# Kernel optimization log

Hardware: AMD Instinct MI355X
Metric: run time of the kernel (lower is better)

## Reference

```python
import jax, jax.numpy as jnp
import numpy as np

H, T, D = 16, 4096, 64
N_SEQ = 8  # packed sequences -> cu_seqlens has N_SEQ+1 entries


def setup_inputs() -> dict:
    key = jax.random.key(0)
    kq, kk, kv, kc = jax.random.split(key, 4)
    q = jax.random.normal(kq, (1, H, T, D), dtype=jnp.float32)
    k = jax.random.normal(kk, (1, H, T, D), dtype=jnp.float32)
    v = jax.random.normal(kv, (1, H, T, D), dtype=jnp.float32)
    # cu_seqlens: monotonically increasing offsets, starts at 0, ends at T
    interior = jnp.sort(jax.random.randint(kc, (N_SEQ - 1,), 1, T, dtype=jnp.int32))
    cu_seqlens = jnp.concatenate([
        jnp.zeros((1,), jnp.int32), interior, jnp.full((1,), T, jnp.int32)
    ])
    return {"q": q, "k": k, "v": v, "cu_seqlens": cu_seqlens}


def reference(q, k, v, cu_seqlens):
    # Faithful to flash_attn_varlen_func(..., causal=False) on packed sequences:
    # non-causal attention restricted block-diagonally to each segment.
    scale = 1.0 / jnp.sqrt(jnp.asarray(D, q.dtype))
    # segment id for every token position
    pos = jnp.arange(T)
    seg = jnp.searchsorted(cu_seqlens[1:], pos, side="right")  # [T]
    mask = seg[:, None] == seg[None, :]                         # [T, T] block-diagonal
    # scores: [1, H, T, T]
    scores = jnp.einsum("bhqd,bhkd->bhqk", q, k) * scale
    neg = jnp.asarray(jnp.finfo(scores.dtype).min, scores.dtype)
    scores = jnp.where(mask[None, None], scores, neg)
    attn = jax.nn.softmax(scores, axis=-1)
    out = jnp.einsum("bhqk,bhkd->bhqd", attn, v)  # [1, H, T, D]
    return out
```

## Files before the change

### kernel.cpp

```cpp
#include <hip/hip_runtime.h>

#define HH 16
#define TT 4096
#define DD 64

typedef __attribute__((ext_vector_type(2))) __fp16 half2r;
typedef __attribute__((ext_vector_type(4))) _Float16 half4;
typedef __attribute__((ext_vector_type(8))) _Float16 half8;
typedef __attribute__((ext_vector_type(2))) float float2v;
typedef __attribute__((ext_vector_type(4))) float float4v;

__global__ __launch_bounds__(256, 4) void pa_fwd(
    const float* __restrict__ qg, const float* __restrict__ kg,
    const float* __restrict__ vg, const int* __restrict__ cu,
    float* __restrict__ outg)
{
    __shared__ __align__(16) _Float16 Kl[2][64 * 64];
    __shared__ __align__(16) _Float16 Vl[2][64 * 64];

    const int tid  = threadIdx.x;
    const int lane = tid & 63;
    const int wave = tid >> 6;
    const int lr   = lane & 15;
    const int lg   = lane >> 4;

    const int bswz = ((int)blockIdx.x & 7) * 128 + ((int)blockIdx.x >> 3);
    const int h    = bswz >> 6;
    const int qblk = (bswz & 63) << 6;
    const int q    = qblk + wave * 16 + lr;

    int s = 0;
    while (cu[s + 1] <= q) ++s;
    const int lo = cu[s], hi = cu[s + 1];

    int sb = 0;
    while (cu[sb + 1] <= qblk) ++sb;
    const int blo = cu[sb];
    while (cu[sb + 1] <= qblk + 63) ++sb;
    const int bhi = cu[sb + 1];

    const int wlo = __shfl(lo, 0);
    const int whi = __shfl(hi, 15);
    const int mlo = __shfl(lo, 15);
    const int mhi = __shfl(hi, 0);

    const float qscale = 0.125f * 1.44269504088896f;
    const float* qrow = qg + ((size_t)h * TT + q) * DD;
    half8 qf8[2];
#pragma unroll
    for (int ds = 0; ds < 2; ++ds) {
        const float* qp = qrow + ds * 32 + lg * 8;
        float4v a = *(const float4v*)qp;
        float4v b = *(const float4v*)(qp + 4);
        half2r p0 = __builtin_amdgcn_cvt_pkrtz(a[0] * qscale, a[1] * qscale);
        half2r p1 = __builtin_amdgcn_cvt_pkrtz(a[2] * qscale, a[3] * qscale);
        half2r p2 = __builtin_amdgcn_cvt_pkrtz(b[0] * qscale, b[1] * qscale);
        half2r p3 = __builtin_amdgcn_cvt_pkrtz(b[2] * qscale, b[3] * qscale);
        qf8[ds][0] = (_Float16)p0[0]; qf8[ds][1] = (_Float16)p0[1];
        qf8[ds][2] = (_Float16)p1[0]; qf8[ds][3] = (_Float16)p1[1];
        qf8[ds][4] = (_Float16)p2[0]; qf8[ds][5] = (_Float16)p2[1];
        qf8[ds][6] = (_Float16)p3[0]; qf8[ds][7] = (_Float16)p3[1];
    }

    const float* kh_ = kg + (size_t)h * TT * DD;
    const float* vh_ = vg + (size_t)h * TT * DD;

    const int srow = tid >> 2;
    const int sc   = tid & 3;
    const unsigned kwrA = (unsigned)(srow * 128 + (((2 * sc)     ^ (srow & 7)) << 4));
    const unsigned kwrB = (unsigned)(srow * 128 + (((2 * sc + 1) ^ (srow & 7)) << 4));
    const int vd2 = tid & 31;
    const int vko = tid >> 5;
    const int vr0 = 2 * vd2, vr1 = 2 * vd2 + 1;
    const unsigned vwrA = (unsigned)(vr0 * 128 + ((vko ^ (vr0 & 7)) << 4));
    const unsigned vwrB = (unsigned)(vr1 * 128 + ((vko ^ (vr1 & 7)) << 4));

    const unsigned kb0 = (unsigned)(lr * 128 + (((lg)     ^ (lr & 7)) << 4));
    const unsigned kb1 = (unsigned)(lr * 128 + (((4 + lg) ^ (lr & 7)) << 4));
    unsigned vrb[4];
#pragma unroll
    for (int t = 0; t < 4; ++t)
        vrb[t] = (unsigned)(lr * 128 + (((2 * t + (lg >> 1)) ^ (lr & 7)) << 4) +
                            ((lg & 1) << 3));

    half4 onesv;
    onesv[0] = onesv[1] = onesv[2] = onesv[3] = (_Float16)1.0f;

    float4v kq[4];
    float2v vv2[8];
    const int t0k = blo & ~63;
    const float4v* kp = (const float4v*)(kh_ + (size_t)(t0k + srow) * DD + sc * 16);
    const float*   vp = vh_ + (size_t)(t0k + vko * 8) * DD + vd2 * 2;

#define ISSUE()                                                                \
    {                                                                          \
        kq[0] = kp[0]; kq[1] = kp[1]; kq[2] = kp[2]; kq[3] = kp[3];            \
        kp += (64 * DD) / 4;                                                   \
        _Pragma("unroll")                                                      \
        for (int c = 0; c < 8; ++c) vv2[c] = *(const float2v*)(vp + c * DD);   \
        vp += 64 * DD;                                                         \
    }

    ISSUE();

    float4v acc[4];
#pragma unroll
    for (int dt = 0; dt < 4; ++dt) acc[dt] = (float4v){0.f, 0.f, 0.f, 0.f};
    float4v acc_l = (float4v){0.f, 0.f, 0.f, 0.f};
    float m_run = -1e30f;

    int cur = 0;
    for (int kt = t0k; kt < bhi; kt += 64) {
        {
            char* Kb = (char*)Kl[cur];
            char* Vb = (char*)Vl[cur];
            half8 hk0, hk1, hv0, hv1;
#pragma unroll
            for (int i = 0; i < 2; ++i) {
                half2r a = __builtin_amdgcn_cvt_pkrtz(kq[i][0], kq[i][1]);
                half2r b = __builtin_amdgcn_cvt_pkrtz(kq[i][2], kq[i][3]);
                hk0[4 * i + 0] = (_Float16)a[0]; hk0[4 * i + 1] = (_Float16)a[1];
                hk0[4 * i + 2] = (_Float16)b[0]; hk0[4 * i + 3] = (_Float16)b[1];
                half2r c2 = __builtin_amdgcn_cvt_pkrtz(kq[2 + i][0], kq[2 + i][1]);
                half2r d2 = __builtin_amdgcn_cvt_pkrtz(kq[2 + i][2], kq[2 + i][3]);
                hk1[4 * i + 0] = (_Float16)c2[0]; hk1[4 * i + 1] = (_Float16)c2[1];
                hk1[4 * i + 2] = (_Float16)d2[0]; hk1[4 * i + 3] = (_Float16)d2[1];
            }
#pragma unroll
            for (int i = 0; i < 4; ++i) {
                half2r a = __builtin_amdgcn_cvt_pkrtz(vv2[2 * i][0], vv2[2 * i + 1][0]);
                half2r b = __builtin_amdgcn_cvt_pkrtz(vv2[2 * i][1], vv2[2 * i + 1][1]);
                hv0[2 * i] = (_Float16)a[0]; hv0[2 * i + 1] = (_Float16)a[1];
                hv1[2 * i] = (_Float16)b[0]; hv1[2 * i + 1] = (_Float16)b[1];
            }
            *(half8*)(Kb + kwrA) = hk0;
            *(half8*)(Kb + kwrB) = hk1;
            *(half8*)(Vb + vwrA) = hv0;
            *(half8*)(Vb + vwrB) = hv1;
        }
        __syncthreads();

        if (kt + 64 < bhi) ISSUE();

        if (!(kt + 64 <= wlo || kt >= whi)) {
            const char* Kb = (const char*)Kl[cur];
            const char* Vb = (const char*)Vl[cur];

            float st[4][4];
            const bool fullv = (kt >= mlo) && (kt + 64 <= mhi);
            __builtin_amdgcn_s_setprio(1);
#pragma unroll
            for (int t = 0; t < 4; ++t) {
                float4v sa = (float4v){0.f, 0.f, 0.f, 0.f};
                half8 kf0 = *(const half8*)(Kb + kb0 + t * 2048);
                half8 kf1 = *(const half8*)(Kb + kb1 + t * 2048);
                sa = __builtin_amdgcn_mfma_f32_16x16x32_f16(kf0, qf8[0], sa, 0, 0, 0);
                sa = __builtin_amdgcn_mfma_f32_16x16x32_f16(kf1, qf8[1], sa, 0, 0, 0);
                if (fullv) {
#pragma unroll
                    for (int j = 0; j < 4; ++j) st[t][j] = sa[j];
                } else {
#pragma unroll
                    for (int j = 0; j < 4; ++j) {
                        const int key = kt + t * 16 + lg * 4 + j;
                        st[t][j] = (key >= lo && key < hi) ? sa[j] : -1e30f;
                    }
                }
            }
            __builtin_amdgcn_s_setprio(0);

            float lmax = fmaxf(fmaxf(st[0][0], st[0][1]), fmaxf(st[0][2], st[0][3]));
            lmax = fmaxf(lmax, fmaxf(fmaxf(st[1][0], st[1][1]), fmaxf(st[1][2], st[1][3])));
            lmax = fmaxf(lmax, fmaxf(fmaxf(st[2][0], st[2][1]), fmaxf(st[2][2], st[2][3])));
            lmax = fmaxf(lmax, fmaxf(fmaxf(st[3][0], st[3][1]), fmaxf(st[3][2], st[3][3])));

            if (__any(lmax > m_run + 11.54f)) {
                float tx = fmaxf(lmax, __shfl_xor(lmax, 16));
                tx = fmaxf(tx, __shfl_xor(tx, 32));
                const float mn = fmaxf(m_run, tx);
                const float a  = exp2f(m_run - mn);
#pragma unroll
                for (int dt = 0; dt < 4; ++dt)
#pragma unroll
                    for (int j = 0; j < 4; ++j) acc[dt][j] *= a;
#pragma unroll
                for (int j = 0; j < 4; ++j) acc_l[j] *= a;
                m_run = mn;
            }

            half4 pb[4];
#pragma unroll
            for (int t = 0; t < 4; ++t) {
                float e0 = exp2f(st[t][0] - m_run);
                float e1 = exp2f(st[t][1] - m_run);
                float e2 = exp2f(st[t][2] - m_run);
                float e3 = exp2f(st[t][3] - m_run);
                half2r a = __builtin_amdgcn_cvt_pkrtz(e0, e1);
                half2r b = __builtin_amdgcn_cvt_pkrtz(e2, e3);
                pb[t][0] = (_Float16)a[0]; pb[t][1] = (_Float16)a[1];
                pb[t][2] = (_Float16)b[0]; pb[t][3] = (_Float16)b[1];
            }

            __builtin_amdgcn_s_setprio(1);
#pragma unroll
            for (int t = 0; t < 4; ++t) {
#pragma unroll
                for (int dt = 0; dt < 4; ++dt) {
                    half4 vf = *(const half4*)(Vb + vrb[t] + dt * 2048);
                    acc[dt] = __builtin_amdgcn_mfma_f32_16x16x16f16(vf, pb[t], acc[dt], 0, 0, 0);
                }
                acc_l = __builtin_amdgcn_mfma_f32_16x16x16f16(onesv, pb[t], acc_l, 0, 0, 0);
            }
            __builtin_amdgcn_s_setprio(0);
        }
        cur ^= 1;
    }

    const float inv = 1.0f / acc_l[0];
    float* orow = outg + ((size_t)h * TT + q) * DD;
#pragma unroll
    for (int dt = 0; dt < 4; ++dt) {
        float4v o;
#pragma unroll
        for (int j = 0; j < 4; ++j) o[j] = acc[dt][j] * inv;
        *(float4v*)(orow + dt * 16 + lg * 4) = o;
    }
#undef ISSUE
}

extern "C" void kernel_launch(void* const* d_in, const int* in_sizes, int n_in,
                              void* d_out, int out_size, void* d_ws, size_t ws_size,
                              hipStream_t stream) {
    const float* q  = (const float*)d_in[0];
    const float* k  = (const float*)d_in[1];
    const float* v  = (const float*)d_in[2];
    const int*   cu = (const int*)d_in[3];
    float* out = (float*)d_out;

    dim3 grid(HH * (TT / 64));
    dim3 block(256);
    hipLaunchKernelGGL(pa_fwd, grid, block, 0, stream, q, k, v, cu, out);
}
```

Measured before the change: 85.65 us.

## Restructure V global loads and LDS layout, prefetch half of V fragments early

The V staging now has each thread load single scalars at column vd2 and vd2+32 rather than float2 pairs, packs them into half4 chunks, and writes them with a new swizzle that also XORs the 8-byte half-slot by a row bit. The V fragment read offsets are updated to match. The first two V fragment groups are read from LDS before the softmax math so their latency overlaps with the exp and max work. This trades wider global loads for narrower scalar ones and adds register pressure for the prefetched fragments, which may matter at 4 blocks per CU.

Result: faster. 81.31 us (-5.1%).

```diff
diff --git a/kernel.cpp b/kernel.cpp
--- a/kernel.cpp
+++ b/kernel.cpp
@@ -7,7 +7,6 @@
 typedef __attribute__((ext_vector_type(2))) __fp16 half2r;
 typedef __attribute__((ext_vector_type(4))) _Float16 half4;
 typedef __attribute__((ext_vector_type(8))) _Float16 half8;
-typedef __attribute__((ext_vector_type(2))) float float2v;
 typedef __attribute__((ext_vector_type(4))) float float4v;
 
 __global__ __launch_bounds__(256, 4) void pa_fwd(
@@ -71,9 +70,12 @@
     const unsigned kwrB = (unsigned)(srow * 128 + (((2 * sc + 1) ^ (srow & 7)) << 4));
     const int vd2 = tid & 31;
     const int vko = tid >> 5;
-    const int vr0 = 2 * vd2, vr1 = 2 * vd2 + 1;
-    const unsigned vwrA = (unsigned)(vr0 * 128 + ((vko ^ (vr0 & 7)) << 4));
-    const unsigned vwrB = (unsigned)(vr1 * 128 + ((vko ^ (vr1 & 7)) << 4));
+    const int vslot = vko ^ (vd2 & 7);
+    const int vhb   = (vd2 >> 3) & 1;
+    const unsigned vwA0 = (unsigned)(vd2 * 128 + vslot * 16 + 8 * vhb);
+    const unsigned vwA1 = (unsigned)(vd2 * 128 + vslot * 16 + 8 * (1 ^ vhb));
+    const unsigned vwB0 = vwA0 + 32 * 128;
+    const unsigned vwB1 = vwA1 + 32 * 128;
 
     const unsigned kb0 = (unsigned)(lr * 128 + (((lg)     ^ (lr & 7)) << 4));
     const unsigned kb1 = (unsigned)(lr * 128 + (((4 + lg) ^ (lr & 7)) << 4));
@@ -81,23 +83,26 @@
 #pragma unroll
     for (int t = 0; t < 4; ++t)
         vrb[t] = (unsigned)(lr * 128 + (((2 * t + (lg >> 1)) ^ (lr & 7)) << 4) +
-                            ((lg & 1) << 3));
+                            (((lg & 1) ^ ((lr >> 3) & 1)) << 3));
 
     half4 onesv;
     onesv[0] = onesv[1] = onesv[2] = onesv[3] = (_Float16)1.0f;
 
     float4v kq[4];
-    float2v vv2[8];
+    float vvA[8], vvB[8];
     const int t0k = blo & ~63;
     const float4v* kp = (const float4v*)(kh_ + (size_t)(t0k + srow) * DD + sc * 16);
-    const float*   vp = vh_ + (size_t)(t0k + vko * 8) * DD + vd2 * 2;
+    const float*   vp = vh_ + (size_t)(t0k + vko * 8) * DD + vd2;
 
 #define ISSUE()                                                                \
     {                                                                          \
         kq[0] = kp[0]; kq[1] = kp[1]; kq[2] = kp[2]; kq[3] = kp[3];            \
         kp += (64 * DD) / 4;                                                   \
         _Pragma("unroll")                                                      \
-        for (int c = 0; c < 8; ++c) vv2[c] = *(const float2v*)(vp + c * DD);   \
+        for (int c = 0; c < 8; ++c) {                                          \
+            vvA[c] = vp[c * DD];                                               \
+            vvB[c] = vp[c * DD + 32];                                          \
+        }                                                                      \
         vp += 64 * DD;                                                         \
     }
 
@@ -114,7 +119,7 @@
         {
             char* Kb = (char*)Kl[cur];
             char* Vb = (char*)Vl[cur];
-            half8 hk0, hk1, hv0, hv1;
+            half8 hk0, hk1;
 #pragma unroll
             for (int i = 0; i < 2; ++i) {
                 half2r a = __builtin_amdgcn_cvt_pkrtz(kq[i][0], kq[i][1]);
@@ -126,17 +131,32 @@
                 hk1[4 * i + 0] = (_Float16)c2[0]; hk1[4 * i + 1] = (_Float16)c2[1];
                 hk1[4 * i + 2] = (_Float16)d2[0]; hk1[4 * i + 3] = (_Float16)d2[1];
             }
-#pragma unroll
-            for (int i = 0; i < 4; ++i) {
-                half2r a = __builtin_amdgcn_cvt_pkrtz(vv2[2 * i][0], vv2[2 * i + 1][0]);
-                half2r b = __builtin_amdgcn_cvt_pkrtz(vv2[2 * i][1], vv2[2 * i + 1][1]);
-                hv0[2 * i] = (_Float16)a[0]; hv0[2 * i + 1] = (_Float16)a[1];
-                hv1[2 * i] = (_Float16)b[0]; hv1[2 * i + 1] = (_Float16)b[1];
-            }
             *(half8*)(Kb + kwrA) = hk0;
             *(half8*)(Kb + kwrB) = hk1;
-            *(half8*)(Vb + vwrA) = hv0;
-            *(half8*)(Vb + vwrB) = hv1;
+
+            half4 uA0, uA1, uB0, uB1;
+            {
+                half2r a = __builtin_amdgcn_cvt_pkrtz(vvA[0], vvA[1]);
+                half2r b = __builtin_amdgcn_cvt_pkrtz(vvA[2], vvA[3]);
+                uA0[0] = (_Float16)a[0]; uA0[1] = (_Float16)a[1];
+                uA0[2] = (_Float16)b[0]; uA0[3] = (_Float16)b[1];
+                half2r c2 = __builtin_amdgcn_cvt_pkrtz(vvA[4], vvA[5]);
+                half2r d2 = __builtin_amdgcn_cvt_pkrtz(vvA[6], vvA[7]);
+                uA1[0] = (_Float16)c2[0]; uA1[1] = (_Float16)c2[1];
+                uA1[2] = (_Float16)d2[0]; uA1[3] = (_Float16)d2[1];
+                half2r e = __builtin_amdgcn_cvt_pkrtz(vvB[0], vvB[1]);
+                half2r f = __builtin_amdgcn_cvt_pkrtz(vvB[2], vvB[3]);
+                uB0[0] = (_Float16)e[0]; uB0[1] = (_Float16)e[1];
+                uB0[2] = (_Float16)f[0]; uB0[3] = (_Float16)f[1];
+                half2r g = __builtin_amdgcn_cvt_pkrtz(vvB[4], vvB[5]);
+                half2r k2 = __builtin_amdgcn_cvt_pkrtz(vvB[6], vvB[7]);
+                uB1[0] = (_Float16)g[0]; uB1[1] = (_Float16)g[1];
+                uB1[2] = (_Float16)k2[0]; uB1[3] = (_Float16)k2[1];
+            }
+            *(half4*)(Vb + vwA0) = uA0;
+            *(half4*)(Vb + vwA1) = uA1;
+            *(half4*)(Vb + vwB0) = uB0;
+            *(half4*)(Vb + vwB1) = uB1;
         }
         __syncthreads();
 
@@ -168,6 +188,13 @@
                 }
             }
             __builtin_amdgcn_s_setprio(0);
+
+            half4 vf01[2][4];
+#pragma unroll
+            for (int t = 0; t < 2; ++t)
+#pragma unroll
+                for (int dt = 0; dt < 4; ++dt)
+                    vf01[t][dt] = *(const half4*)(Vb + vrb[t] + dt * 2048);
 
             float lmax = fmaxf(fmaxf(st[0][0], st[0][1]), fmaxf(st[0][2], st[0][3]));
             lmax = fmaxf(lmax, fmaxf(fmaxf(st[1][0], st[1][1]), fmaxf(st[1][2], st[1][3])));
@@ -203,7 +230,14 @@
 
             __builtin_amdgcn_s_setprio(1);
 #pragma unroll
-            for (int t = 0; t < 4; ++t) {
+            for (int t = 0; t < 2; ++t) {
+#pragma unroll
+                for (int dt = 0; dt < 4; ++dt)
+                    acc[dt] = __builtin_amdgcn_mfma_f32_16x16x16f16(vf01[t][dt], pb[t], acc[dt], 0, 0, 0);
+                acc_l = __builtin_amdgcn_mfma_f32_16x16x16f16(onesv, pb[t], acc_l, 0, 0, 0);
+            }
+#pragma unroll
+            for (int t = 2; t < 4; ++t) {
 #pragma unroll
                 for (int dt = 0; dt < 4; ++dt) {
                     half4 vf = *(const half4*)(Vb + vrb[t] + dt * 2048);
```

## Software-pipeline QK of next tile with softmax/PV of current tile

Applied to the files above, without the earlier changes.

Restructures the main loop so the QK^T MFMAs for tile kt+64 are issued before the softmax and PV work for tile kt, with scores carried across iterations. This exposes more independent MFMA work per wave to hide latency. It also changes the V global load and LDS write pattern to scalar loads with a new half-swizzled layout, and relaxes launch bounds from 4 to 2 blocks per CU to allow more registers. The cost is higher register pressure, possibly lower occupancy, and an extra barrier per iteration.

Measured after the change: 95.06 us. 11.0% more time.

```diff
diff --git a/kernel.cpp b/kernel.cpp
--- a/kernel.cpp
+++ b/kernel.cpp
@@ -7,10 +7,9 @@
 typedef __attribute__((ext_vector_type(2))) __fp16 half2r;
 typedef __attribute__((ext_vector_type(4))) _Float16 half4;
 typedef __attribute__((ext_vector_type(8))) _Float16 half8;
-typedef __attribute__((ext_vector_type(2))) float float2v;
 typedef __attribute__((ext_vector_type(4))) float float4v;
 
-__global__ __launch_bounds__(256, 4) void pa_fwd(
+__global__ __launch_bounds__(256, 2) void pa_fwd(
     const float* __restrict__ qg, const float* __restrict__ kg,
     const float* __restrict__ vg, const int* __restrict__ cu,
     float* __restrict__ outg)
@@ -71,9 +70,12 @@
     const unsigned kwrB = (unsigned)(srow * 128 + (((2 * sc + 1) ^ (srow & 7)) << 4));
     const int vd2 = tid & 31;
     const int vko = tid >> 5;
-    const int vr0 = 2 * vd2, vr1 = 2 * vd2 + 1;
-    const unsigned vwrA = (unsigned)(vr0 * 128 + ((vko ^ (vr0 & 7)) << 4));
-    const unsigned vwrB = (unsigned)(vr1 * 128 + ((vko ^ (vr1 & 7)) << 4));
+    const int vslot = vko ^ (vd2 & 7);
+    const int vhb   = (vd2 >> 3) & 1;
+    const unsigned vwA0 = (unsigned)(vd2 * 128 + vslot * 16 + 8 * vhb);
+    const unsigned vwA1 = (unsigned)(vd2 * 128 + vslot * 16 + 8 * (1 ^ vhb));
+    const unsigned vwB0 = vwA0 + 32 * 128;
+    const unsigned vwB1 = vwA1 + 32 * 128;
 
     const unsigned kb0 = (unsigned)(lr * 128 + (((lg)     ^ (lr & 7)) << 4));
     const unsigned kb1 = (unsigned)(lr * 128 + (((4 + lg) ^ (lr & 7)) << 4));
@@ -81,27 +83,98 @@
 #pragma unroll
     for (int t = 0; t < 4; ++t)
         vrb[t] = (unsigned)(lr * 128 + (((2 * t + (lg >> 1)) ^ (lr & 7)) << 4) +
-                            ((lg & 1) << 3));
+                            (((lg & 1) ^ ((lr >> 3) & 1)) << 3));
 
     half4 onesv;
     onesv[0] = onesv[1] = onesv[2] = onesv[3] = (_Float16)1.0f;
 
     float4v kq[4];
-    float2v vv2[8];
-    const int t0k = blo & ~63;
+    float vvA[8], vvB[8];
+    const int t0k  = blo & ~63;
+    const int tend = bhi;
     const float4v* kp = (const float4v*)(kh_ + (size_t)(t0k + srow) * DD + sc * 16);
-    const float*   vp = vh_ + (size_t)(t0k + vko * 8) * DD + vd2 * 2;
+    const float*   vp = vh_ + (size_t)(t0k + vko * 8) * DD + vd2;
 
 #define ISSUE()                                                                \
     {                                                                          \
         kq[0] = kp[0]; kq[1] = kp[1]; kq[2] = kp[2]; kq[3] = kp[3];            \
         kp += (64 * DD) / 4;                                                   \
         _Pragma("unroll")                                                      \
-        for (int c = 0; c < 8; ++c) vv2[c] = *(const float2v*)(vp + c * DD);   \
+        for (int c = 0; c < 8; ++c) {                                          \
+            vvA[c] = vp[c * DD];                                               \
+            vvB[c] = vp[c * DD + 32];                                          \
+        }                                                                      \
         vp += 64 * DD;                                                         \
     }
 
-    ISSUE();
+#define PACKW(CUR)                                                             \
+    {                                                                          \
+        char* Kb = (char*)Kl[CUR];                                             \
+        char* Vb = (char*)Vl[CUR];                                             \
+        half8 hk0, hk1;                                                        \
+        _Pragma("unroll")                                                      \
+        for (int i = 0; i < 2; ++i) {                                          \
+            half2r a = __builtin_amdgcn_cvt_pkrtz(kq[i][0], kq[i][1]);         \
+            half2r b = __builtin_amdgcn_cvt_pkrtz(kq[i][2], kq[i][3]);         \
+            hk0[4*i+0] = (_Float16)a[0]; hk0[4*i+1] = (_Float16)a[1];          \
+            hk0[4*i+2] = (_Float16)b[0]; hk0[4*i+3] = (_Float16)b[1];          \
+            half2r c2 = __builtin_amdgcn_cvt_pkrtz(kq[2+i][0], kq[2+i][1]);    \
+            half2r d2 = __builtin_amdgcn_cvt_pkrtz(kq[2+i][2], kq[2+i][3]);    \
+            hk1[4*i+0] = (_Float16)c2[0]; hk1[4*i+1] = (_Float16)c2[1];        \
+            hk1[4*i+2] = (_Float16)d2[0]; hk1[4*i+3] = (_Float16)d2[1];        \
+        }                                                                      \
+        *(half8*)(Kb + kwrA) = hk0;                                            \
+        *(half8*)(Kb + kwrB) = hk1;                                            \
+        half4 uA0, uA1, uB0, uB1;                                              \
+        {                                                                      \
+            half2r a = __builtin_amdgcn_cvt_pkrtz(vvA[0], vvA[1]);             \
+            half2r b = __builtin_amdgcn_cvt_pkrtz(vvA[2], vvA[3]);             \
+            uA0[0] = (_Float16)a[0]; uA0[1] = (_Float16)a[1];                  \
+            uA0[2] = (_Float16)b[0]; uA0[3] = (_Float16)b[1];                  \
+            half2r c2 = __builtin_amdgcn_cvt_pkrtz(vvA[4], vvA[5]);            \
+            half2r d2 = __builtin_amdgcn_cvt_pkrtz(vvA[6], vvA[7]);            \
+            uA1[0] = (_Float16)c2[0]; uA1[1] = (_Float16)c2[1];                \
+            uA1[2] = (_Float16)d2[0]; uA1[3] = (_Float16)d2[1];                \
+            half2r e = __builtin_amdgcn_cvt_pkrtz(vvB[0], vvB[1]);             \
+            half2r f = __builtin_amdgcn_cvt_pkrtz(vvB[2], vvB[3]);             \
+            uB0[0] = (_Float16)e[0]; uB0[1] = (_Float16)e[1];                  \
+            uB0[2] = (_Float16)f[0]; uB0[3] = (_Float16)f[1];                  \
+            half2r g = __builtin_amdgcn_cvt_pkrtz(vvB[4], vvB[5]);             \
+            half2r k2 = __builtin_amdgcn_cvt_pkrtz(vvB[6], vvB[7]);            \
+            uB1[0] = (_Float16)g[0]; uB1[1] = (_Float16)g[1];                  \
+            uB1[2] = (_Float16)k2[0]; uB1[3] = (_Float16)k2[1];                \
+        }                                                                      \
+        *(half4*)(Vb + vwA0) = uA0;                                            \
+        *(half4*)(Vb + vwA1) = uA1;                                            \
+        *(half4*)(Vb + vwB0) = uB0;                                            \
+        *(half4*)(Vb + vwB1) = uB1;                                            \
+    }
+
+#define QKM(KT, BUF, ST, VALID)                                                \
+    if (VALID) {                                                               \
+        const char* Kb_ = (const char*)Kl[BUF];                                \
+        const bool fullv_ = ((KT) >= mlo) && ((KT) + 64 <= mhi);               \
+        __builtin_amdgcn_s_setprio(1);                                         \
+        _Pragma("unroll")                                                      \
+        for (int t = 0; t < 4; ++t) {                                          \
+            float4v sa = (float4v){0.f, 0.f, 0.f, 0.f};                        \
+            half8 kf0 = *(const half8*)(Kb_ + kb0 + t * 2048);                 \
+            half8 kf1 = *(const half8*)(Kb_ + kb1 + t * 2048);                 \
+            sa = __builtin_amdgcn_mfma_f32_16x16x32_f16(kf0, qf8[0], sa, 0, 0, 0); \
+            sa = __builtin_amdgcn_mfma_f32_16x16x32_f16(kf1, qf8[1], sa, 0, 0, 0); \
+            if (fullv_) {                                                      \
+                _Pragma("unroll")                                              \
+                for (int j = 0; j < 4; ++j) ST[t][j] = sa[j];                  \
+            } else {                                                           \
+                _Pragma("unroll")                                              \
+                for (int j = 0; j < 4; ++j) {                                  \
+                    const int key = (KT) + t * 16 + lg * 4 + j;                \
+                    ST[t][j] = (key >= lo && key < hi) ? sa[j] : -1e30f;       \
+                }                                                              \
+            }                                                                  \
+        }                                                                      \
+        __builtin_amdgcn_s_setprio(0);                                         \
+    }
 
     float4v acc[4];
 #pragma unroll
@@ -109,65 +182,28 @@
     float4v acc_l = (float4v){0.f, 0.f, 0.f, 0.f};
     float m_run = -1e30f;
 
+    ISSUE();
+    PACKW(0);
+    if (t0k + 64 < tend) ISSUE();
+    __syncthreads();
+    float st[4][4];
+    bool cv = !(t0k + 64 <= wlo || t0k >= whi);
+    QKM(t0k, 0, st, cv);
+
     int cur = 0;
-    for (int kt = t0k; kt < bhi; kt += 64) {
-        {
-            char* Kb = (char*)Kl[cur];
-            char* Vb = (char*)Vl[cur];
-            half8 hk0, hk1, hv0, hv1;
-#pragma unroll
-            for (int i = 0; i < 2; ++i) {
-                half2r a = __builtin_amdgcn_cvt_pkrtz(kq[i][0], kq[i][1]);
-                half2r b = __builtin_amdgcn_cvt_pkrtz(kq[i][2], kq[i][3]);
-                hk0[4 * i + 0] = (_Float16)a[0]; hk0[4 * i + 1] = (_Float16)a[1];
-                hk0[4 * i + 2] = (_Float16)b[0]; hk0[4 * i + 3] = (_Float16)b[1];
-                half2r c2 = __builtin_amdgcn_cvt_pkrtz(kq[2 + i][0], kq[2 + i][1]);
-                half2r d2 = __builtin_amdgcn_cvt_pkrtz(kq[2 + i][2], kq[2 + i][3]);
-                hk1[4 * i + 0] = (_Float16)c2[0]; hk1[4 * i + 1] = (_Float16)c2[1];
-                hk1[4 * i + 2] = (_Float16)d2[0]; hk1[4 * i + 3] = (_Float16)d2[1];
-            }
-#pragma unroll
-            for (int i = 0; i < 4; ++i) {
-                half2r a = __builtin_amdgcn_cvt_pkrtz(vv2[2 * i][0], vv2[2 * i + 1][0]);
-                half2r b = __builtin_amdgcn_cvt_pkrtz(vv2[2 * i][1], vv2[2 * i + 1][1]);
-                hv0[2 * i] = (_Float16)a[0]; hv0[2 * i + 1] = (_Float16)a[1];
-                hv1[2 * i] = (_Float16)b[0]; hv1[2 * i + 1] = (_Float16)b[1];
-            }
-            *(half8*)(Kb + kwrA) = hk0;
-            *(half8*)(Kb + kwrB) = hk1;
-            *(half8*)(Vb + vwrA) = hv0;
-            *(half8*)(Vb + vwrB) = hv1;
-        }
+    for (int kt = t0k; kt < tend; kt += 64) {
         __syncthreads();
-
-        if (kt + 64 < bhi) ISSUE();
-
-        if (!(kt + 64 <= wlo || kt >= whi)) {
-            const char* Kb = (const char*)Kl[cur];
+        if (kt + 64 < tend) PACKW(cur ^ 1);
+        if (kt + 128 < tend) ISSUE();
+        __syncthreads();
+
+        const bool nxv = (kt + 64 < tend) &&
+                         !(kt + 128 <= wlo || kt + 64 >= whi);
+        float stn[4][4];
+        QKM(kt + 64, cur ^ 1, stn, nxv);
+
+        if (cv) {
             const char* Vb = (const char*)Vl[cur];
-
-            float st[4][4];
-            const bool fullv = (kt >= mlo) && (kt + 64 <= mhi);
-            __builtin_amdgcn_s_setprio(1);
-#pragma unroll
-            for (int t = 0; t < 4; ++t) {
-                float4v sa = (float4v){0.f, 0.f, 0.f, 0.f};
-                half8 kf0 = *(const half8*)(Kb + kb0 + t * 2048);
-                half8 kf1 = *(const half8*)(Kb + kb1 + t * 2048);
-                sa = __builtin_amdgcn_mfma_f32_16x16x32_f16(kf0, qf8[0], sa, 0, 0, 0);
-                sa = __builtin_amdgcn_mfma_f32_16x16x32_f16(kf1, qf8[1], sa, 0, 0, 0);
-                if (fullv) {
-#pragma unroll
-                    for (int j = 0; j < 4; ++j) st[t][j] = sa[j];
-                } else {
-#pragma unroll
-                    for (int j = 0; j < 4; ++j) {
-                        const int key = kt + t * 16 + lg * 4 + j;
-                        st[t][j] = (key >= lo && key < hi) ? sa[j] : -1e30f;
-                    }
-                }
-            }
-            __builtin_amdgcn_s_setprio(0);
 
             float lmax = fmaxf(fmaxf(st[0][0], st[0][1]), fmaxf(st[0][2], st[0][3]));
             lmax = fmaxf(lmax, fmaxf(fmaxf(st[1][0], st[1][1]), fmaxf(st[1][2], st[1][3])));
@@ -213,6 +249,14 @@
             }
             __builtin_amdgcn_s_setprio(0);
         }
+
+        if (nxv) {
+#pragma unroll
+            for (int t = 0; t < 4; ++t)
+#pragma unroll
+                for (int j = 0; j < 4; ++j) st[t][j] = stn[t][j];
+        }
+        cv = nxv;
         cur ^= 1;
     }
 
@@ -226,6 +270,8 @@
         *(float4v*)(orow + dt * 16 + lg * 4) = o;
     }
 #undef ISSUE
+#undef PACKW
+#undef QKM
 }
 
 extern "C" void kernel_launch(void* const* d_in, const int* in_sizes, int n_in,
```

## Precompute swizzled fp16 K/V in a prep kernel and stream it into LDS

Applied to the files above, without the earlier changes.

Adds a prep kernel that converts K and V from fp32 to fp16 once. It writes them to workspace already in the swizzled LDS tile layout, with V transposed. The attention kernel then copies 16-byte chunks straight into shared memory, with no per-tile conversion and half the bytes per K/V tile load. The first half of the V fragments is also loaded before the softmax so the LDS reads overlap the exp work. The cost is an extra kernel launch and a workspace write and read pass.

Result: faster. 80.64 us (-5.8%).

```diff
diff --git a/kernel.cpp b/kernel.cpp
--- a/kernel.cpp
+++ b/kernel.cpp
@@ -7,12 +7,83 @@
 typedef __attribute__((ext_vector_type(2))) __fp16 half2r;
 typedef __attribute__((ext_vector_type(4))) _Float16 half4;
 typedef __attribute__((ext_vector_type(8))) _Float16 half8;
-typedef __attribute__((ext_vector_type(2))) float float2v;
 typedef __attribute__((ext_vector_type(4))) float float4v;
 
+__global__ __launch_bounds__(256) void pa_prep(
+    const float* __restrict__ kg, const float* __restrict__ vg,
+    _Float16* __restrict__ k16, _Float16* __restrict__ v16)
+{
+    __shared__ __align__(16) float Kf[64 * 68];
+    __shared__ __align__(16) float Vf[64 * 65];
+
+    const int bid  = blockIdx.x;
+    const int h    = bid >> 6;
+    const int tile = bid & 63;
+    const int kt   = tile << 6;
+    const int t    = threadIdx.x;
+
+    const int row = t >> 2, c4 = (t & 3) * 16;
+    const float* ksrc = kg + ((size_t)(h * TT) + kt + row) * DD + c4;
+    const float* vsrc = vg + ((size_t)(h * TT) + kt + row) * DD + c4;
+#pragma unroll
+    for (int i = 0; i < 4; ++i) {
+        *(float4v*)&Kf[row * 68 + c4 + i * 4] = *(const float4v*)(ksrc + i * 4);
+        *(float4v*)&Vf[row * 65 + c4 + i * 4] = *(const float4v*)(vsrc + i * 4);
+    }
+    __syncthreads();
+
+    char* kdst = (char*)k16 + ((size_t)h * 64 + tile) * 8192;
+    char* vdst = (char*)v16 + ((size_t)h * 64 + tile) * 8192;
+
+#pragma unroll
+    for (int rep = 0; rep < 2; ++rep) {
+        const int idx = t + rep * 256;
+        const int r = idx >> 3, s = idx & 7;
+        {
+            const int sc = s ^ (r & 7);
+            float4v a = *(const float4v*)&Kf[r * 68 + sc * 8];
+            float4v b = *(const float4v*)&Kf[r * 68 + sc * 8 + 4];
+            half2r p0 = __builtin_amdgcn_cvt_pkrtz(a[0], a[1]);
+            half2r p1 = __builtin_amdgcn_cvt_pkrtz(a[2], a[3]);
+            half2r p2 = __builtin_amdgcn_cvt_pkrtz(b[0], b[1]);
+            half2r p3 = __builtin_amdgcn_cvt_pkrtz(b[2], b[3]);
+            half8 hk;
+            hk[0] = (_Float16)p0[0]; hk[1] = (_Float16)p0[1];
+            hk[2] = (_Float16)p1[0]; hk[3] = (_Float16)p1[1];
+            hk[4] = (_Float16)p2[0]; hk[5] = (_Float16)p2[1];
+            hk[6] = (_Float16)p3[0]; hk[7] = (_Float16)p3[1];
+            *(half8*)(kdst + r * 128 + s * 16) = hk;
+        }
+        {
+            const int e  = s ^ (r & 7);
+            const int rb = (r >> 3) & 1;
+            const int k0 = 8 * e + 4 * rb;
+            const int k1 = 8 * e + 4 * (1 - rb);
+            float x0 = Vf[(k0 + 0) * 65 + r];
+            float x1 = Vf[(k0 + 1) * 65 + r];
+            float x2 = Vf[(k0 + 2) * 65 + r];
+            float x3 = Vf[(k0 + 3) * 65 + r];
+            float y0 = Vf[(k1 + 0) * 65 + r];
+            float y1 = Vf[(k1 + 1) * 65 + r];
+            float y2 = Vf[(k1 + 2) * 65 + r];
+            float y3 = Vf[(k1 + 3) * 65 + r];
+            half2r p0 = __builtin_amdgcn_cvt_pkrtz(x0, x1);
+            half2r p1 = __builtin_amdgcn_cvt_pkrtz(x2, x3);
+            half2r p2 = __builtin_amdgcn_cvt_pkrtz(y0, y1);
+            half2r p3 = __builtin_amdgcn_cvt_pkrtz(y2, y3);
+            half8 hv;
+            hv[0] = (_Float16)p0[0]; hv[1] = (_Float16)p0[1];
+            hv[2] = (_Float16)p1[0]; hv[3] = (_Float16)p1[1];
+            hv[4] = (_Float16)p2[0]; hv[5] = (_Float16)p2[1];
+            hv[6] = (_Float16)p3[0]; hv[7] = (_Float16)p3[1];
+            *(half8*)(vdst + r * 128 + s * 16) = hv;
+        }
+    }
+}
+
 __global__ __launch_bounds__(256, 4) void pa_fwd(
-    const float* __restrict__ qg, const float* __restrict__ kg,
-    const float* __restrict__ vg, const int* __restrict__ cu,
+    const float* __restrict__ qg, const _Float16* __restrict__ k16,
+    const _Float16* __restrict__ v16, const int* __restrict__ cu,
     float* __restrict__ outg)
 {
     __shared__ __align__(16) _Float16 Kl[2][64 * 64];
@@ -62,18 +133,8 @@
         qf8[ds][6] = (_Float16)p3[0]; qf8[ds][7] = (_Float16)p3[1];
     }
 
-    const float* kh_ = kg + (size_t)h * TT * DD;
-    const float* vh_ = vg + (size_t)h * TT * DD;
-
-    const int srow = tid >> 2;
-    const int sc   = tid & 3;
-    const unsigned kwrA = (unsigned)(srow * 128 + (((2 * sc)     ^ (srow & 7)) << 4));
-    const unsigned kwrB = (unsigned)(srow * 128 + (((2 * sc + 1) ^ (srow & 7)) << 4));
-    const int vd2 = tid & 31;
-    const int vko = tid >> 5;
-    const int vr0 = 2 * vd2, vr1 = 2 * vd2 + 1;
-    const unsigned vwrA = (unsigned)(vr0 * 128 + ((vko ^ (vr0 & 7)) << 4));
-    const unsigned vwrB = (unsigned)(vr1 * 128 + ((vko ^ (vr1 & 7)) << 4));
+    const unsigned soff0 = (unsigned)(wave * 2048 + lane * 16);
+    const unsigned soff1 = soff0 + 1024;
 
     const unsigned kb0 = (unsigned)(lr * 128 + (((lg)     ^ (lr & 7)) << 4));
     const unsigned kb1 = (unsigned)(lr * 128 + (((4 + lg) ^ (lr & 7)) << 4));
@@ -81,24 +142,21 @@
 #pragma unroll
     for (int t = 0; t < 4; ++t)
         vrb[t] = (unsigned)(lr * 128 + (((2 * t + (lg >> 1)) ^ (lr & 7)) << 4) +
-                            ((lg & 1) << 3));
+                            (((lg & 1) ^ ((lr >> 3) & 1)) << 3));
 
     half4 onesv;
     onesv[0] = onesv[1] = onesv[2] = onesv[3] = (_Float16)1.0f;
 
-    float4v kq[4];
-    float2v vv2[8];
+    half8 kr0, kr1, vr0, vr1;
     const int t0k = blo & ~63;
-    const float4v* kp = (const float4v*)(kh_ + (size_t)(t0k + srow) * DD + sc * 16);
-    const float*   vp = vh_ + (size_t)(t0k + vko * 8) * DD + vd2 * 2;
+    const char* gk = (const char*)k16 + (size_t)h * 524288 + (size_t)t0k * 128 + soff0;
+    const char* gv = (const char*)v16 + (size_t)h * 524288 + (size_t)t0k * 128 + soff0;
 
 #define ISSUE()                                                                \
     {                                                                          \
-        kq[0] = kp[0]; kq[1] = kp[1]; kq[2] = kp[2]; kq[3] = kp[3];            \
-        kp += (64 * DD) / 4;                                                   \
-        _Pragma("unroll")                                                      \
-        for (int c = 0; c < 8; ++c) vv2[c] = *(const float2v*)(vp + c * DD);   \
-        vp += 64 * DD;                                                         \
+        kr0 = *(const half8*)gk; kr1 = *(const half8*)(gk + 1024);             \
+        vr0 = *(const half8*)gv; vr1 = *(const half8*)(gv + 1024);             \
+        gk += 8192; gv += 8192;                                                \
     }
 
     ISSUE();
@@ -114,29 +172,10 @@
         {
             char* Kb = (char*)Kl[cur];
             char* Vb = (char*)Vl[cur];
-            half8 hk0, hk1, hv0, hv1;
-#pragma unroll
-            for (int i = 0; i < 2; ++i) {
-                half2r a = __builtin_amdgcn_cvt_pkrtz(kq[i][0], kq[i][1]);
-                half2r b = __builtin_amdgcn_cvt_pkrtz(kq[i][2], kq[i][3]);
-                hk0[4 * i + 0] = (_Float16)a[0]; hk0[4 * i + 1] = (_Float16)a[1];
-                hk0[4 * i + 2] = (_Float16)b[0]; hk0[4 * i + 3] = (_Float16)b[1];
-                half2r c2 = __builtin_amdgcn_cvt_pkrtz(kq[2 + i][0], kq[2 + i][1]);
-                half2r d2 = __builtin_amdgcn_cvt_pkrtz(kq[2 + i][2], kq[2 + i][3]);
-                hk1[4 * i + 0] = (_Float16)c2[0]; hk1[4 * i + 1] = (_Float16)c2[1];
-                hk1[4 * i + 2] = (_Float16)d2[0]; hk1[4 * i + 3] = (_Float16)d2[1];
-            }
-#pragma unroll
-            for (int i = 0; i < 4; ++i) {
-                half2r a = __builtin_amdgcn_cvt_pkrtz(vv2[2 * i][0], vv2[2 * i + 1][0]);
-                half2r b = __builtin_amdgcn_cvt_pkrtz(vv2[2 * i][1], vv2[2 * i + 1][1]);
-                hv0[2 * i] = (_Float16)a[0]; hv0[2 * i + 1] = (_Float16)a[1];
-                hv1[2 * i] = (_Float16)b[0]; hv1[2 * i + 1] = (_Float16)b[1];
-            }
-            *(half8*)(Kb + kwrA) = hk0;
-            *(half8*)(Kb + kwrB) = hk1;
-            *(half8*)(Vb + vwrA) = hv0;
-            *(half8*)(Vb + vwrB) = hv1;
+            *(half8*)(Kb + soff0) = kr0;
+            *(half8*)(Kb + soff1) = kr1;
+            *(half8*)(Vb + soff0) = vr0;
+            *(half8*)(Vb + soff1) = vr1;
         }
         __syncthreads();
 
@@ -168,6 +207,13 @@
                 }
             }
             __builtin_amdgcn_s_setprio(0);
+
+            half4 vf01[2][4];
+#pragma unroll
+            for (int t = 0; t < 2; ++t)
+#pragma unroll
+                for (int dt = 0; dt < 4; ++dt)
+                    vf01[t][dt] = *(const half4*)(Vb + vrb[t] + dt * 2048);
 
             float lmax = fmaxf(fmaxf(st[0][0], st[0][1]), fmaxf(st[0][2], st[0][3]));
             lmax = fmaxf(lmax, fmaxf(fmaxf(st[1][0], st[1][1]), fmaxf(st[1][2], st[1][3])));
@@ -203,7 +249,14 @@
 
             __builtin_amdgcn_s_setprio(1);
 #pragma unroll
-            for (int t = 0; t < 4; ++t) {
+            for (int t = 0; t < 2; ++t) {
+#pragma unroll
+                for (int dt = 0; dt < 4; ++dt)
+                    acc[dt] = __builtin_amdgcn_mfma_f32_16x16x16f16(vf01[t][dt], pb[t], acc[dt], 0, 0, 0);
+                acc_l = __builtin_amdgcn_mfma_f32_16x16x16f16(onesv, pb[t], acc_l, 0, 0, 0);
+            }
+#pragma unroll
+            for (int t = 2; t < 4; ++t) {
 #pragma unroll
                 for (int dt = 0; dt < 4; ++dt) {
                     half4 vf = *(const half4*)(Vb + vrb[t] + dt * 2048);
@@ -237,7 +290,12 @@
     const int*   cu = (const int*)d_in[3];
     float* out = (float*)d_out;
 
-    dim3 grid(HH * (TT / 64));
-    dim3 block(256);
-    hipLaunchKernelGGL(pa_fwd, grid, block, 0, stream, q, k, v, cu, out);
+    _Float16* k16 = (_Float16*)d_ws;
+    _Float16* v16 = (_Float16*)((char*)d_ws + 8388608);
+
+    dim3 pgrid(HH * 64), pblock(256);
+    hipLaunchKernelGGL(pa_prep, pgrid, pblock, 0, stream, k, v, k16, v16);
+
+    dim3 grid(HH * (TT / 64)), block(256);
+    hipLaunchKernelGGL(pa_fwd, grid, block, 0, stream, q, k16, v16, cu, out);
 }
```
